# Kernel optimization log

Hardware: AMD Instinct MI355X
Metric: run time of the kernel (lower is better)

The kernel has to match this reference:

```python
import jax, jax.numpy as jnp
import numpy as np

T, N, E, D = 4, 50000, 800000, 256
VOCAB = 64000


def _gcn_layer(x, row, col, w, W, b, n):
    # PyG GCNConv: add self-loops (weight 1), symmetric normalization on
    # weighted in-degree (target/col), h = x @ W, scatter-add, then + bias.
    loops = jnp.arange(n, dtype=row.dtype)
    row2 = jnp.concatenate([row, loops])
    col2 = jnp.concatenate([col, loops])
    w2 = jnp.concatenate([w, jnp.ones((n,), x.dtype)])
    deg = jax.ops.segment_sum(w2, col2, num_segments=n)
    dinv = jnp.where(deg > 0, jax.lax.rsqrt(deg), 0.0)
    norm = dinv[row2] * w2 * dinv[col2]              # [E+N]
    h = x @ W                                        # [N, D]
    out = jax.ops.segment_sum(norm[:, None] * h[row2], col2, num_segments=n)
    return out + b


def _encode_timestep(ids, row, col, w, emb, W1, b1, W2, b2, W3, b3):
    x = emb[ids]                                     # [N, D] embedding lookup
    x = _gcn_layer(x, row, col, w, W1, b1, ids.shape[0])
    x = _gcn_layer(x, row, col, w, W2, b2, ids.shape[0])
    x = _gcn_layer(x, row, col, w, W3, b3, ids.shape[0])
    return x


def setup_inputs() -> dict:
    key = jax.random.key(0)
    ks = jax.random.split(key, 8)
    scale = 1.0 / np.sqrt(D)
    return {
        "node_features": jax.random.randint(ks[0], (T, N), 0, VOCAB, dtype=jnp.int32),
        "edge_index": jax.random.randint(ks[1], (T, 2, E), 0, N, dtype=jnp.int32),
        "edge_weight": jax.random.uniform(ks[2], (T, E), dtype=jnp.float32),
        "emb": jax.random.normal(ks[3], (VOCAB, D), dtype=jnp.float32),
        "W1": jax.random.normal(ks[4], (D, D), dtype=jnp.float32) * scale,
        "b1": jnp.zeros((D,), jnp.float32),
        "W2": jax.random.normal(ks[5], (D, D), dtype=jnp.float32) * scale,
        "b2": jnp.zeros((D,), jnp.float32),
        "W3": jax.random.normal(ks[6], (D, D), dtype=jnp.float32) * scale,
        "b3": jnp.zeros((D,), jnp.float32),
    }


def reference(node_features, edge_index, edge_weight, emb, W1, b1, W2, b2, W3, b3):
    outs = []
    for t in range(node_features.shape[0]):  # fixed small timestep count
        outs.append(_encode_timestep(node_features[t], edge_index[t, 0],
                                     edge_index[t, 1], edge_weight[t],
                                     emb, W1, b1, W2, b2, W3, b3))
    return jnp.concatenate(outs, axis=0)  # [T*N, D]
```

## Files before the change

kernel.cpp:

```cpp
#include <hip/hip_runtime.h>

#define T_STEPS 4
#define NN 50000
#define EE 800000
#define DD 256
#define VOCAB 64000
#define NB ((NN + 255) / 256)

typedef __attribute__((ext_vector_type(8))) short short8;
typedef __attribute__((ext_vector_type(4))) float floatx4;

__device__ __forceinline__ unsigned short f2bf(float f) {
    unsigned u = __float_as_uint(f);
    return (unsigned short)((u + 0x7FFFu + ((u >> 16) & 1u)) >> 16);
}
__device__ __forceinline__ float bf2f(unsigned short s) {
    return __uint_as_float(((unsigned)s) << 16);
}

__device__ __forceinline__ void async16(const unsigned short* g, unsigned short* l) {
    __builtin_amdgcn_global_load_lds(
        (const __attribute__((address_space(1))) void*)g,
        (__attribute__((address_space(3))) void*)l, 16, 0, 0);
}

__global__ __launch_bounds__(256) void init_deg_cnt(float* __restrict__ deg,
                                                    int* __restrict__ cnt, int n) {
    int i = blockIdx.x * 256 + threadIdx.x;
    if (i < n) { deg[i] = 1.0f; cnt[i] = 0; }
}

__global__ __launch_bounds__(256) void edge_deg_cnt(const int* __restrict__ col,
                                                    const float* __restrict__ w,
                                                    float* __restrict__ deg,
                                                    int* __restrict__ cnt, int e) {
    int i = blockIdx.x * 256 + threadIdx.x;
    if (i < e) {
        int c = col[i];
        atomicAdd(&deg[c], w[i]);
        atomicAdd(&cnt[c], 1);
    }
}

__global__ __launch_bounds__(256) void compute_dinv(const float* __restrict__ deg,
                                                    float* __restrict__ dinv, int n) {
    int i = blockIdx.x * 256 + threadIdx.x;
    if (i < n) {
        float d = deg[i];
        dinv[i] = d > 0.0f ? rsqrtf(d) : 0.0f;
    }
}

__global__ __launch_bounds__(256) void block_sums(const int* __restrict__ cnt,
                                                  int* __restrict__ bsum, int n) {
    __shared__ int sm[256];
    int i = blockIdx.x * 256 + threadIdx.x;
    sm[threadIdx.x] = (i < n) ? cnt[i] : 0;
    __syncthreads();
    for (int s = 128; s > 0; s >>= 1) {
        if ((int)threadIdx.x < s) sm[threadIdx.x] += sm[threadIdx.x + s];
        __syncthreads();
    }
    if (threadIdx.x == 0) bsum[blockIdx.x] = sm[0];
}

__global__ __launch_bounds__(256) void scan_bsum(const int* __restrict__ bsum,
                                                 int* __restrict__ boff, int nb) {
    __shared__ int sm[256];
    int v = ((int)threadIdx.x < nb) ? bsum[threadIdx.x] : 0;
    sm[threadIdx.x] = v;
    __syncthreads();
    for (int o = 1; o < 256; o <<= 1) {
        int t = (threadIdx.x >= (unsigned)o) ? sm[threadIdx.x - o] : 0;
        __syncthreads();
        sm[threadIdx.x] += t;
        __syncthreads();
    }
    if ((int)threadIdx.x < nb) boff[threadIdx.x] = sm[threadIdx.x] - v;
}

__global__ __launch_bounds__(256) void scan_final(const int* __restrict__ cnt,
                                                  const int* __restrict__ boff,
                                                  int* __restrict__ colptr,
                                                  int* __restrict__ next, int n, int e) {
    __shared__ int sm[256];
    int i = blockIdx.x * 256 + threadIdx.x;
    int v = (i < n) ? cnt[i] : 0;
    sm[threadIdx.x] = v;
    __syncthreads();
    for (int o = 1; o < 256; o <<= 1) {
        int t = (threadIdx.x >= (unsigned)o) ? sm[threadIdx.x - o] : 0;
        __syncthreads();
        sm[threadIdx.x] += t;
        __syncthreads();
    }
    int excl = sm[threadIdx.x] - v + boff[blockIdx.x];
    if (i < n) { colptr[i] = excl; next[i] = excl; }
    if (i == 0) colptr[n] = e;
}

__global__ __launch_bounds__(256) void fill_csr(const int* __restrict__ row,
                                                const int* __restrict__ col,
                                                const float* __restrict__ w,
                                                const float* __restrict__ dinv,
                                                int* __restrict__ next,
                                                int* __restrict__ srow,
                                                float* __restrict__ snorm, int e) {
    int i = blockIdx.x * 256 + threadIdx.x;
    if (i < e) {
        int r = row[i], c = col[i];
        int p = atomicAdd(&next[c], 1);
        srow[p] = r;
        snorm[p] = dinv[r] * w[i] * dinv[c];
    }
}

__global__ __launch_bounds__(256) void s1_kernel(const int* __restrict__ colptr,
                                                 const float* __restrict__ snorm,
                                                 const float* __restrict__ dinv,
                                                 float* __restrict__ s1, int n) {
    int c = blockIdx.x * 256 + threadIdx.x;
    if (c < n) {
        float di = dinv[c];
        float s = di * di;
        int p1 = colptr[c + 1];
        for (int p = colptr[c]; p < p1; ++p) s += snorm[p];
        s1[c] = s;
    }
}

__global__ __launch_bounds__(256) void s2_kernel(const int* __restrict__ colptr,
                                                 const int* __restrict__ srow,
                                                 const float* __restrict__ snorm,
                                                 const float* __restrict__ dinv,
                                                 const float* __restrict__ s1,
                                                 float* __restrict__ s2, int n) {
    int c = blockIdx.x * 256 + threadIdx.x;
    if (c < n) {
        float di = dinv[c];
        float s = di * di * s1[c];
        int p1 = colptr[c + 1];
        for (int p = colptr[c]; p < p1; ++p) s += snorm[p] * s1[srow[p]];
        s2[c] = s;
    }
}

__global__ __launch_bounds__(256) void matmul256(const float* __restrict__ A,
                                                 const float* __restrict__ B,
                                                 float* __restrict__ C) {
    __shared__ float arow[256];
    int i = blockIdx.x, j = threadIdx.x;
    arow[j] = A[i * 256 + j];
    __syncthreads();
    float acc = 0.f;
#pragma unroll 8
    for (int k = 0; k < 256; ++k) acc += arow[k] * B[k * 256 + j];
    C[i * 256 + j] = acc;
}

__global__ __launch_bounds__(256) void matvec256(const float* __restrict__ x,
                                                 const float* __restrict__ W,
                                                 float* __restrict__ y) {
    __shared__ float xs[256];
    int j = threadIdx.x;
    xs[j] = x[j];
    __syncthreads();
    float acc = 0.f;
#pragma unroll 8
    for (int k = 0; k < 256; ++k) acc += xs[k] * W[k * 256 + j];
    y[j] = acc;
}

__global__ __launch_bounds__(256) void convert_wc(const float* __restrict__ Wc,
                                                  unsigned short* __restrict__ wt) {
    int n = blockIdx.x;
    int k = threadIdx.x;
    wt[n * 256 + k] = f2bf(Wc[k * 256 + n]);
}

__global__ __launch_bounds__(256) void convert_emb(const float* __restrict__ emb,
                                                   unsigned short* __restrict__ ebf,
                                                   int total4) {
    int t = blockIdx.x * 256 + threadIdx.x;
    if (t < total4) {
        float4 v = ((const float4*)emb)[t];
        ushort4 o;
        o.x = f2bf(v.x); o.y = f2bf(v.y); o.z = f2bf(v.z); o.w = f2bf(v.w);
        ((ushort4*)ebf)[t] = o;
    }
}

__global__ __launch_bounds__(256) void mfma_gemm(const int* __restrict__ ids,
                                                 const unsigned short* __restrict__ ebf,
                                                 const unsigned short* __restrict__ wt,
                                                 unsigned short* __restrict__ h2,
                                                 int M) {
    __shared__ __align__(16) unsigned short As[128 * 32];
    __shared__ __align__(16) unsigned short Bs[128 * 32];

    int tid = threadIdx.x;
    int lane = tid & 63;
    int wave = tid >> 6;
    int row0 = blockIdx.y * 128;
    int col0 = blockIdx.x * 128;
    int wm = (wave & 1) * 64;
    int wn = (wave >> 1) * 64;
    int quad = lane >> 4;
    int cl = lane & 15;

    int idx0 = tid, idx1 = 256 + tid;
    int c0 = idx0 >> 7, m0 = idx0 & 127;
    int c1 = idx1 >> 7;
    int gr0 = row0 + m0; if (gr0 >= M) gr0 = M - 1;
    int id0 = ids[gr0];
    const unsigned short* srcA0 = ebf + (size_t)id0 * 256 + c0 * 8;
    const unsigned short* srcA1 = ebf + (size_t)id0 * 256 + c1 * 8;
    const unsigned short* srcB0 = wt + (size_t)(col0 + m0) * 256 + c0 * 8;
    const unsigned short* srcB1 = wt + (size_t)(col0 + m0) * 256 + c1 * 8;
    unsigned short* dstA0 = As + idx0 * 8;
    unsigned short* dstA1 = As + idx1 * 8;
    unsigned short* dstB0 = Bs + idx0 * 8;
    unsigned short* dstB1 = Bs + idx1 * 8;

    floatx4 acc[4][4] = {};

    for (int k0 = 0; k0 < 256; k0 += 32) {
        if (k0) __syncthreads();
        async16(srcA0 + k0, dstA0);
        async16(srcA1 + k0, dstA1);
        async16(srcB0 + k0, dstB0);
        async16(srcB1 + k0, dstB1);
        __syncthreads();

        short8 af[4], bfr[4];
#pragma unroll
        for (int i = 0; i < 4; ++i)
            af[i] = *(const short8*)&As[(quad * 128 + wm + i * 16 + cl) * 8];
#pragma unroll
        for (int j = 0; j < 4; ++j)
            bfr[j] = *(const short8*)&Bs[(quad * 128 + wn + j * 16 + cl) * 8];
#pragma unroll
        for (int i = 0; i < 4; ++i)
#pragma unroll
            for (int j = 0; j < 4; ++j)
                acc[i][j] = __builtin_amdgcn_mfma_f32_16x16x32_bf16(
                    af[i], bfr[j], acc[i][j], 0, 0, 0);
    }

#pragma unroll
    for (int i = 0; i < 4; ++i) {
#pragma unroll
        for (int r = 0; r < 4; ++r) {
            int gr = row0 + wm + i * 16 + quad * 4 + r;
            if (gr < M) {
                size_t base = (size_t)gr * 256 + col0 + wn + cl;
#pragma unroll
                for (int j = 0; j < 4; ++j)
                    h2[base + j * 16] = f2bf(acc[i][j][r]);
            }
        }
    }
}

__global__ __launch_bounds__(256) void agg_kernel(const unsigned short* __restrict__ h2,
                                                  const int* __restrict__ colptr,
                                                  const int* __restrict__ srow,
                                                  const float* __restrict__ snorm,
                                                  const float* __restrict__ dinv,
                                                  const float* __restrict__ s1,
                                                  const float* __restrict__ s2,
                                                  const float* __restrict__ v1,
                                                  const float* __restrict__ v2,
                                                  const float* __restrict__ b3,
                                                  float* __restrict__ dstf,
                                                  unsigned short* __restrict__ dstb,
                                                  int n) {
    int wave = threadIdx.x >> 6;
    int lane = threadIdx.x & 63;
    int c = blockIdx.x * 4 + wave;
    if (c >= n) return;
    int p0 = colptr[c];
    int p1 = colptr[c + 1];
    float di = dinv[c];
    float self = di * di;

    const ushort4* h4 = (const ushort4*)h2;
    int cbase = c * 64 + lane;

    ushort4 sv = h4[cbase];
    float ax = self * bf2f(sv.x), ay = self * bf2f(sv.y);
    float az = self * bf2f(sv.z), aw = self * bf2f(sv.w);
    float bx = 0.f, by = 0.f, bz = 0.f, bw = 0.f;

    int j = p0;
    for (; j + 1 < p1; j += 2) {
        int r0 = srow[j];
        int r1 = srow[j + 1];
        float w0 = snorm[j];
        float w1 = snorm[j + 1];
        ushort4 v0 = h4[(size_t)r0 * 64 + lane];
        ushort4 v1q = h4[(size_t)r1 * 64 + lane];
        ax += w0 * bf2f(v0.x); ay += w0 * bf2f(v0.y);
        az += w0 * bf2f(v0.z); aw += w0 * bf2f(v0.w);
        bx += w1 * bf2f(v1q.x); by += w1 * bf2f(v1q.y);
        bz += w1 * bf2f(v1q.z); bw += w1 * bf2f(v1q.w);
    }
    if (j < p1) {
        int r0 = srow[j];
        float w0 = snorm[j];
        ushort4 v0 = h4[(size_t)r0 * 64 + lane];
        ax += w0 * bf2f(v0.x); ay += w0 * bf2f(v0.y);
        az += w0 * bf2f(v0.z); aw += w0 * bf2f(v0.w);
    }
    float ox = ax + bx, oy = ay + by, oz = az + bz, ow = aw + bw;
    if (dstb) {
        ushort4 o;
        o.x = f2bf(ox); o.y = f2bf(oy); o.z = f2bf(oz); o.w = f2bf(ow);
        ((ushort4*)dstb)[cbase] = o;
    } else {
        float s1c = s1[c], s2c = s2[c];
        float4 a1 = ((const float4*)v1)[lane];
        float4 a2 = ((const float4*)v2)[lane];
        float4 a3 = ((const float4*)b3)[lane];
        ox += s2c * a1.x + s1c * a2.x + a3.x;
        oy += s2c * a1.y + s1c * a2.y + a3.y;
        oz += s2c * a1.z + s1c * a2.z + a3.z;
        ow += s2c * a1.w + s1c * a2.w + a3.w;
        ((float4*)dstf)[cbase] = make_float4(ox, oy, oz, ow);
    }
}

extern "C" void kernel_launch(void* const* d_in, const int* in_sizes, int n_in,
                              void* d_out, int out_size, void* d_ws, size_t ws_size,
                              hipStream_t stream) {
    const int*   node_features = (const int*)d_in[0];
    const int*   edge_index    = (const int*)d_in[1];
    const float* edge_weight   = (const float*)d_in[2];
    const float* emb           = (const float*)d_in[3];
    const float* W1 = (const float*)d_in[4];
    const float* b1 = (const float*)d_in[5];
    const float* W2 = (const float*)d_in[6];
    const float* b2 = (const float*)d_in[7];
    const float* W3 = (const float*)d_in[8];
    const float* b3 = (const float*)d_in[9];
    float* out = (float*)d_out;

    char* ws = (char*)d_ws;
    size_t off = 0;
    auto alloc = [&](size_t bytes) -> void* {
        void* p = ws + off;
        off = (off + bytes + 255) & ~(size_t)255;
        return p;
    };
    unsigned short* ebf    = (unsigned short*)alloc((size_t)VOCAB * DD * 2);
    unsigned short* xb     = (unsigned short*)alloc((size_t)NN * DD * 2);
    unsigned short* h2     = (unsigned short*)alloc((size_t)NN * DD * 2);
    unsigned short* wtc    = (unsigned short*)alloc((size_t)DD * DD * 2);
    float* Wtmp   = (float*)alloc((size_t)DD * DD * 4);
    float* Wc32   = (float*)alloc((size_t)DD * DD * 4);
    float* u      = (float*)alloc((size_t)DD * 4);
    float* v1     = (float*)alloc((size_t)DD * 4);
    float* v2     = (float*)alloc((size_t)DD * 4);
    float* deg    = (float*)alloc((size_t)NN * 4);
    float* dinv   = (float*)alloc((size_t)NN * 4);
    float* s1v    = (float*)alloc((size_t)NN * 4);
    float* s2v    = (float*)alloc((size_t)NN * 4);
    int*   cnt    = (int*)alloc((size_t)NN * 4);
    int*   colptr = (int*)alloc((size_t)(NN + 1) * 4);
    int*   next   = (int*)alloc((size_t)NN * 4);
    int*   srow   = (int*)alloc((size_t)EE * 4);
    float* snorm  = (float*)alloc((size_t)EE * 4);
    int*   bsum   = (int*)alloc((size_t)NB * 4);
    int*   boff   = (int*)alloc((size_t)NB * 4);
    (void)ws_size; (void)n_in; (void)in_sizes; (void)out_size;

    const int gN   = (NN + 255) / 256;
    const int gE   = (EE + 255) / 256;
    const int gAgg = (NN + 3) / 4;
    const int gEmb = (VOCAB * 64 + 255) / 256;
    dim3 gGemm(2, (NN + 127) / 128);

    convert_emb<<<gEmb, 256, 0, stream>>>(emb, ebf, VOCAB * 64);
    matmul256<<<256, 256, 0, stream>>>(W1, W2, Wtmp);
    matmul256<<<256, 256, 0, stream>>>(Wtmp, W3, Wc32);
    convert_wc<<<256, 256, 0, stream>>>(Wc32, wtc);
    matvec256<<<1, 256, 0, stream>>>(b1, W2, u);
    matvec256<<<1, 256, 0, stream>>>(u, W3, v1);
    matvec256<<<1, 256, 0, stream>>>(b2, W3, v2);

    for (int t = 0; t < T_STEPS; ++t) {
        const int*   ids = node_features + (size_t)t * NN;
        const int*   row = edge_index + (size_t)t * 2 * EE;
        const int*   col = row + EE;
        const float* w   = edge_weight + (size_t)t * EE;

        init_deg_cnt<<<gN, 256, 0, stream>>>(deg, cnt, NN);
        edge_deg_cnt<<<gE, 256, 0, stream>>>(col, w, deg, cnt, EE);
        compute_dinv<<<gN, 256, 0, stream>>>(deg, dinv, NN);
        block_sums<<<NB, 256, 0, stream>>>(cnt, bsum, NN);
        scan_bsum<<<1, 256, 0, stream>>>(bsum, boff, NB);
        scan_final<<<NB, 256, 0, stream>>>(cnt, boff, colptr, next, NN, EE);
        fill_csr<<<gE, 256, 0, stream>>>(row, col, w, dinv, next, srow, snorm, EE);

        s1_kernel<<<gN, 256, 0, stream>>>(colptr, snorm, dinv, s1v, NN);
        s2_kernel<<<gN, 256, 0, stream>>>(colptr, srow, snorm, dinv, s1v, s2v, NN);

        mfma_gemm<<<gGemm, 256, 0, stream>>>(ids, ebf, wtc, h2, NN);

        agg_kernel<<<gAgg, 256, 0, stream>>>(h2, colptr, srow, snorm, dinv,
                                             nullptr, nullptr, nullptr, nullptr, nullptr,
                                             nullptr, xb, NN);
        agg_kernel<<<gAgg, 256, 0, stream>>>(xb, colptr, srow, snorm, dinv,
                                             nullptr, nullptr, nullptr, nullptr, nullptr,
                                             nullptr, h2, NN);
        agg_kernel<<<gAgg, 256, 0, stream>>>(h2, colptr, srow, snorm, dinv,
                                             s1v, s2v, v1, v2, b3,
                                             out + (size_t)t * NN * DD, nullptr, NN);
    }
}
```

Baseline: 1.798 ms.

## Fuse CSR preprocessing, pack edges, widen GEMM tile, half-wave edge aggregation

Merges dinv computation with block sums and moves the s1 reduction into fill_csr via atomics. The s2 reduction now runs inside the first aggregation pass, removing two per-node CSR walks. Row index and norm are packed into one int2 per edge, so each edge needs a single load. The GEMM now covers all 256 output columns per block, so each embedding tile is gathered once, at the cost of more accumulators and LDS. Aggregation splits each wave into two halves that take alternating edges with 16-byte loads and combine via shuffle, which adds atomic float-order nondeterminism in s1.

```diff
diff --git a/kernel.cpp b/kernel.cpp
--- a/kernel.cpp
+++ b/kernel.cpp
@@ -42,19 +42,19 @@
     }
 }
 
-__global__ __launch_bounds__(256) void compute_dinv(const float* __restrict__ deg,
-                                                    float* __restrict__ dinv, int n) {
+__global__ __launch_bounds__(256) void dinv_bsums(const float* __restrict__ deg,
+                                                  float* __restrict__ dinv,
+                                                  float* __restrict__ s1,
+                                                  const int* __restrict__ cnt,
+                                                  int* __restrict__ bsum, int n) {
     int i = blockIdx.x * 256 + threadIdx.x;
     if (i < n) {
         float d = deg[i];
-        dinv[i] = d > 0.0f ? rsqrtf(d) : 0.0f;
-    }
-}
-
-__global__ __launch_bounds__(256) void block_sums(const int* __restrict__ cnt,
-                                                  int* __restrict__ bsum, int n) {
+        float r = d > 0.0f ? rsqrtf(d) : 0.0f;
+        dinv[i] = r;
+        s1[i] = r * r;
+    }
     __shared__ int sm[256];
-    int i = blockIdx.x * 256 + threadIdx.x;
     sm[threadIdx.x] = (i < n) ? cnt[i] : 0;
     __syncthreads();
     for (int s = 128; s > 0; s >>= 1) {
@@ -104,44 +104,15 @@
                                                 const float* __restrict__ w,
                                                 const float* __restrict__ dinv,
                                                 int* __restrict__ next,
-                                                int* __restrict__ srow,
-                                                float* __restrict__ snorm, int e) {
+                                                int2* __restrict__ edges,
+                                                float* __restrict__ s1, int e) {
     int i = blockIdx.x * 256 + threadIdx.x;
     if (i < e) {
         int r = row[i], c = col[i];
+        float nm = dinv[r] * w[i] * dinv[c];
         int p = atomicAdd(&next[c], 1);
-        srow[p] = r;
-        snorm[p] = dinv[r] * w[i] * dinv[c];
-    }
-}
-
-__global__ __launch_bounds__(256) void s1_kernel(const int* __restrict__ colptr,
-                                                 const float* __restrict__ snorm,
-                                                 const float* __restrict__ dinv,
-                                                 float* __restrict__ s1, int n) {
-    int c = blockIdx.x * 256 + threadIdx.x;
-    if (c < n) {
-        float di = dinv[c];
-        float s = di * di;
-        int p1 = colptr[c + 1];
-        for (int p = colptr[c]; p < p1; ++p) s += snorm[p];
-        s1[c] = s;
-    }
-}
-
-__global__ __launch_bounds__(256) void s2_kernel(const int* __restrict__ colptr,
-                                                 const int* __restrict__ srow,
-                                                 const float* __restrict__ snorm,
-                                                 const float* __restrict__ dinv,
-                                                 const float* __restrict__ s1,
-                                                 float* __restrict__ s2, int n) {
-    int c = blockIdx.x * 256 + threadIdx.x;
-    if (c < n) {
-        float di = dinv[c];
-        float s = di * di * s1[c];
-        int p1 = colptr[c + 1];
-        for (int p = colptr[c]; p < p1; ++p) s += snorm[p] * s1[srow[p]];
-        s2[c] = s;
+        edges[p] = make_int2(r, __float_as_int(nm));
+        atomicAdd(&s1[c], nm);
     }
 }
 
@@ -196,53 +167,52 @@
                                                  unsigned short* __restrict__ h2,
                                                  int M) {
     __shared__ __align__(16) unsigned short As[128 * 32];
-    __shared__ __align__(16) unsigned short Bs[128 * 32];
+    __shared__ __align__(16) unsigned short Bs[256 * 32];
 
     int tid = threadIdx.x;
     int lane = tid & 63;
     int wave = tid >> 6;
-    int row0 = blockIdx.y * 128;
-    int col0 = blockIdx.x * 128;
+    int row0 = blockIdx.x * 128;
     int wm = (wave & 1) * 64;
-    int wn = (wave >> 1) * 64;
+    int wn = (wave >> 1) * 128;
     int quad = lane >> 4;
     int cl = lane & 15;
 
-    int idx0 = tid, idx1 = 256 + tid;
-    int c0 = idx0 >> 7, m0 = idx0 & 127;
-    int c1 = idx1 >> 7;
-    int gr0 = row0 + m0; if (gr0 >= M) gr0 = M - 1;
-    int id0 = ids[gr0];
-    const unsigned short* srcA0 = ebf + (size_t)id0 * 256 + c0 * 8;
-    const unsigned short* srcA1 = ebf + (size_t)id0 * 256 + c1 * 8;
-    const unsigned short* srcB0 = wt + (size_t)(col0 + m0) * 256 + c0 * 8;
-    const unsigned short* srcB1 = wt + (size_t)(col0 + m0) * 256 + c1 * 8;
-    unsigned short* dstA0 = As + idx0 * 8;
-    unsigned short* dstA1 = As + idx1 * 8;
-    unsigned short* dstB0 = Bs + idx0 * 8;
-    unsigned short* dstB1 = Bs + idx1 * 8;
-
-    floatx4 acc[4][4] = {};
+    int uA0 = tid, uA1 = 256 + tid;
+    int cA0 = uA0 >> 7, mA0 = uA0 & 127;
+    int cA1 = uA1 >> 7;
+    int gr = row0 + mA0; if (gr >= M) gr = M - 1;
+    int id0 = ids[gr];
+    const unsigned short* srcA0 = ebf + (size_t)id0 * 256 + cA0 * 8;
+    const unsigned short* srcA1 = ebf + (size_t)id0 * 256 + cA1 * 8;
+    unsigned short* dstA0 = As + uA0 * 8;
+    unsigned short* dstA1 = As + uA1 * 8;
+
+    const unsigned short* srcB = wt + (size_t)tid * 256;
+    unsigned short* dstBbase = Bs + tid * 8;
+
+    floatx4 acc[4][8] = {};
 
     for (int k0 = 0; k0 < 256; k0 += 32) {
         if (k0) __syncthreads();
         async16(srcA0 + k0, dstA0);
         async16(srcA1 + k0, dstA1);
-        async16(srcB0 + k0, dstB0);
-        async16(srcB1 + k0, dstB1);
-        __syncthreads();
-
-        short8 af[4], bfr[4];
+#pragma unroll
+        for (int s5 = 0; s5 < 4; ++s5)
+            async16(srcB + s5 * 8 + k0, dstBbase + s5 * 2048);
+        __syncthreads();
+
+        short8 af[4], bfr[8];
 #pragma unroll
         for (int i = 0; i < 4; ++i)
             af[i] = *(const short8*)&As[(quad * 128 + wm + i * 16 + cl) * 8];
 #pragma unroll
-        for (int j = 0; j < 4; ++j)
-            bfr[j] = *(const short8*)&Bs[(quad * 128 + wn + j * 16 + cl) * 8];
+        for (int j = 0; j < 8; ++j)
+            bfr[j] = *(const short8*)&Bs[(quad * 256 + wn + j * 16 + cl) * 8];
 #pragma unroll
         for (int i = 0; i < 4; ++i)
 #pragma unroll
-            for (int j = 0; j < 4; ++j)
+            for (int j = 0; j < 8; ++j)
                 acc[i][j] = __builtin_amdgcn_mfma_f32_16x16x32_bf16(
                     af[i], bfr[j], acc[i][j], 0, 0, 0);
     }
@@ -251,11 +221,11 @@
     for (int i = 0; i < 4; ++i) {
 #pragma unroll
         for (int r = 0; r < 4; ++r) {
-            int gr = row0 + wm + i * 16 + quad * 4 + r;
-            if (gr < M) {
-                size_t base = (size_t)gr * 256 + col0 + wn + cl;
-#pragma unroll
-                for (int j = 0; j < 4; ++j)
+            int gr2 = row0 + wm + i * 16 + quad * 4 + r;
+            if (gr2 < M) {
+                size_t base = (size_t)gr2 * 256 + wn + cl;
+#pragma unroll
+                for (int j = 0; j < 8; ++j)
                     h2[base + j * 16] = f2bf(acc[i][j][r]);
             }
         }
@@ -264,10 +234,10 @@
 
 __global__ __launch_bounds__(256) void agg_kernel(const unsigned short* __restrict__ h2,
                                                   const int* __restrict__ colptr,
-                                                  const int* __restrict__ srow,
-                                                  const float* __restrict__ snorm,
+                                                  const int2* __restrict__ edges,
                                                   const float* __restrict__ dinv,
                                                   const float* __restrict__ s1,
+                                                  float* __restrict__ s2_out,
                                                   const float* __restrict__ s2,
                                                   const float* __restrict__ v1,
                                                   const float* __restrict__ v2,
@@ -277,56 +247,80 @@
                                                   int n) {
     int wave = threadIdx.x >> 6;
     int lane = threadIdx.x & 63;
+    int h = lane >> 5;
+    int s = lane & 31;
     int c = blockIdx.x * 4 + wave;
     if (c >= n) return;
     int p0 = colptr[c];
     int p1 = colptr[c + 1];
     float di = dinv[c];
     float self = di * di;
-
-    const ushort4* h4 = (const ushort4*)h2;
-    int cbase = c * 64 + lane;
-
-    ushort4 sv = h4[cbase];
-    float ax = self * bf2f(sv.x), ay = self * bf2f(sv.y);
-    float az = self * bf2f(sv.z), aw = self * bf2f(sv.w);
-    float bx = 0.f, by = 0.f, bz = 0.f, bw = 0.f;
-
-    int j = p0;
-    for (; j + 1 < p1; j += 2) {
-        int r0 = srow[j];
-        int r1 = srow[j + 1];
-        float w0 = snorm[j];
-        float w1 = snorm[j + 1];
-        ushort4 v0 = h4[(size_t)r0 * 64 + lane];
-        ushort4 v1q = h4[(size_t)r1 * 64 + lane];
-        ax += w0 * bf2f(v0.x); ay += w0 * bf2f(v0.y);
-        az += w0 * bf2f(v0.z); aw += w0 * bf2f(v0.w);
-        bx += w1 * bf2f(v1q.x); by += w1 * bf2f(v1q.y);
-        bz += w1 * bf2f(v1q.z); bw += w1 * bf2f(v1q.w);
+    bool do_s2 = (s2_out != nullptr);
+
+    float accA[8] = {}, accB[8] = {};
+    float ssA = 0.f, ssB = 0.f;
+
+    if (h == 0) {
+        short8 v = *(const short8*)(h2 + (size_t)c * 256 + s * 8);
+#pragma unroll
+        for (int k = 0; k < 8; ++k) accA[k] += self * bf2f((unsigned short)v[k]);
+    }
+
+    int j = p0 + h;
+    for (; j + 2 < p1; j += 4) {
+        int2 e0 = edges[j];
+        int2 e1 = edges[j + 2];
+        float w0 = __int_as_float(e0.y);
+        float w1 = __int_as_float(e1.y);
+        short8 va = *(const short8*)(h2 + (size_t)e0.x * 256 + s * 8);
+        short8 vb = *(const short8*)(h2 + (size_t)e1.x * 256 + s * 8);
+        if (do_s2) { ssA += w0 * s1[e0.x]; ssB += w1 * s1[e1.x]; }
+#pragma unroll
+        for (int k = 0; k < 8; ++k) {
+            accA[k] += w0 * bf2f((unsigned short)va[k]);
+            accB[k] += w1 * bf2f((unsigned short)vb[k]);
+        }
     }
     if (j < p1) {
-        int r0 = srow[j];
-        float w0 = snorm[j];
-        ushort4 v0 = h4[(size_t)r0 * 64 + lane];
-        ax += w0 * bf2f(v0.x); ay += w0 * bf2f(v0.y);
-        az += w0 * bf2f(v0.z); aw += w0 * bf2f(v0.w);
-    }
-    float ox = ax + bx, oy = ay + by, oz = az + bz, ow = aw + bw;
+        int2 e0 = edges[j];
+        float w0 = __int_as_float(e0.y);
+        short8 va = *(const short8*)(h2 + (size_t)e0.x * 256 + s * 8);
+        if (do_s2) ssA += w0 * s1[e0.x];
+#pragma unroll
+        for (int k = 0; k < 8; ++k) accA[k] += w0 * bf2f((unsigned short)va[k]);
+    }
+
+    float tot[8];
+#pragma unroll
+    for (int k = 0; k < 8; ++k) {
+        float o = accA[k] + accB[k];
+        tot[k] = o + __shfl(o, lane ^ 32, 64);
+    }
+    if (do_s2) {
+        float ss = ssA + ssB;
+        ss += __shfl(ss, lane ^ 32, 64);
+        if (lane == 0) s2_out[c] = self * s1[c] + ss;
+    }
+
     if (dstb) {
-        ushort4 o;
-        o.x = f2bf(ox); o.y = f2bf(oy); o.z = f2bf(oz); o.w = f2bf(ow);
-        ((ushort4*)dstb)[cbase] = o;
+        if (h == 0) {
+            short8 o;
+#pragma unroll
+            for (int k = 0; k < 8; ++k) o[k] = (short)f2bf(tot[k]);
+            *(short8*)(dstb + (size_t)c * 256 + s * 8) = o;
+        }
     } else {
-        float s1c = s1[c], s2c = s2[c];
-        float4 a1 = ((const float4*)v1)[lane];
-        float4 a2 = ((const float4*)v2)[lane];
-        float4 a3 = ((const float4*)b3)[lane];
-        ox += s2c * a1.x + s1c * a2.x + a3.x;
-        oy += s2c * a1.y + s1c * a2.y + a3.y;
-        oz += s2c * a1.z + s1c * a2.z + a3.z;
-        ow += s2c * a1.w + s1c * a2.w + a3.w;
-        ((float4*)dstf)[cbase] = make_float4(ox, oy, oz, ow);
+        if (h == 0) {
+            float s1c = s1[c], s2c = s2[c];
+            int f0 = s * 8;
+            float ob[8];
+#pragma unroll
+            for (int k = 0; k < 8; ++k)
+                ob[k] = tot[k] + s2c * v1[f0 + k] + s1c * v2[f0 + k] + b3[f0 + k];
+            float* o = dstf + (size_t)c * 256 + f0;
+            ((float4*)o)[0] = make_float4(ob[0], ob[1], ob[2], ob[3]);
+            ((float4*)o)[1] = make_float4(ob[4], ob[5], ob[6], ob[7]);
+        }
     }
 }
 
@@ -368,8 +362,7 @@
     int*   cnt    = (int*)alloc((size_t)NN * 4);
     int*   colptr = (int*)alloc((size_t)(NN + 1) * 4);
     int*   next   = (int*)alloc((size_t)NN * 4);
-    int*   srow   = (int*)alloc((size_t)EE * 4);
-    float* snorm  = (float*)alloc((size_t)EE * 4);
+    int2*  edges  = (int2*)alloc((size_t)EE * 8);
     int*   bsum   = (int*)alloc((size_t)NB * 4);
     int*   boff   = (int*)alloc((size_t)NB * 4);
     (void)ws_size; (void)n_in; (void)in_sizes; (void)out_size;
@@ -378,7 +371,7 @@
     const int gE   = (EE + 255) / 256;
     const int gAgg = (NN + 3) / 4;
     const int gEmb = (VOCAB * 64 + 255) / 256;
-    dim3 gGemm(2, (NN + 127) / 128);
+    const int gGemm = (NN + 127) / 128;
 
     convert_emb<<<gEmb, 256, 0, stream>>>(emb, ebf, VOCAB * 64);
     matmul256<<<256, 256, 0, stream>>>(W1, W2, Wtmp);
@@ -396,25 +389,21 @@
 
         init_deg_cnt<<<gN, 256, 0, stream>>>(deg, cnt, NN);
         edge_deg_cnt<<<gE, 256, 0, stream>>>(col, w, deg, cnt, EE);
-        compute_dinv<<<gN, 256, 0, stream>>>(deg, dinv, NN);
-        block_sums<<<NB, 256, 0, stream>>>(cnt, bsum, NN);
+        dinv_bsums<<<gN, 256, 0, stream>>>(deg, dinv, s1v, cnt, bsum, NN);
         scan_bsum<<<1, 256, 0, stream>>>(bsum, boff, NB);
-        scan_final<<<NB, 256, 0, stream>>>(cnt, boff, colptr, next, NN, EE);
-        fill_csr<<<gE, 256, 0, stream>>>(row, col, w, dinv, next, srow, snorm, EE);
-
-        s1_kernel<<<gN, 256, 0, stream>>>(colptr, snorm, dinv, s1v, NN);
-        s2_kernel<<<gN, 256, 0, stream>>>(colptr, srow, snorm, dinv, s1v, s2v, NN);
+        scan_final<<<gN, 256, 0, stream>>>(cnt, boff, colptr, next, NN, EE);
+        fill_csr<<<gE, 256, 0, stream>>>(row, col, w, dinv, next, edges, s1v, EE);
 
         mfma_gemm<<<gGemm, 256, 0, stream>>>(ids, ebf, wtc, h2, NN);
 
-        agg_kernel<<<gAgg, 256, 0, stream>>>(h2, colptr, srow, snorm, dinv,
-                                             nullptr, nullptr, nullptr, nullptr, nullptr,
+        agg_kernel<<<gAgg, 256, 0, stream>>>(h2, colptr, edges, dinv,
+                                             s1v, s2v, nullptr, nullptr, nullptr, nullptr,
                                              nullptr, xb, NN);
-        agg_kernel<<<gAgg, 256, 0, stream>>>(xb, colptr, srow, snorm, dinv,
-                                             nullptr, nullptr, nullptr, nullptr, nullptr,
+        agg_kernel<<<gAgg, 256, 0, stream>>>(xb, colptr, edges, dinv,
+                                             nullptr, nullptr, nullptr, nullptr, nullptr, nullptr,
                                              nullptr, h2, NN);
-        agg_kernel<<<gAgg, 256, 0, stream>>>(h2, colptr, srow, snorm, dinv,
-                                             s1v, s2v, v1, v2, b3,
+        agg_kernel<<<gAgg, 256, 0, stream>>>(h2, colptr, edges, dinv,
+                                             s1v, nullptr, s2v, v1, v2, b3,
                                              out + (size_t)t * NN * DD, nullptr, NN);
     }
 }
```

Result: no change. 1.797 ms (-0.1%).
